# Optimization experiments

Measured on AMD Instinct MI355X. Metric: run time of the kernel, lower is better.

Reference implementation:

```python
import jax, jax.numpy as jnp
import numpy as np

# LIF parameters (norse defaults, matching lif_params in init_kwargs)
TAU_MEM_INV = 100.0
TAU_SYN_INV = 200.0
V_LEAK = 0.0
V_TH = 1.0
V_RESET = 0.0
DT = 0.001
POOL = (2, 2)

B, C, H, W = 16, 64, 256, 256


def setup_inputs() -> dict:
    key = jax.random.key(0)
    input_signal = jax.random.normal(key, (B, C, H, W), dtype=jnp.float32)
    membrane = jnp.zeros((B, C, H, W), dtype=jnp.float32)
    synaptic = jnp.zeros((B, C, H, W), dtype=jnp.float32)
    return {"input_signal": input_signal, "membrane": membrane, "synaptic": synaptic}


def reference(input_signal, membrane, synaptic):
    # Single-timestep LIF update per pixel (Euler integration):
    #   i' = i + dt * tau_syn_inv * (-i) + input
    #   v' = v + dt * tau_mem_inv * ((v_leak - v) + i')
    #   spike = v' >= v_th
    i_new = synaptic * (1.0 - DT * TAU_SYN_INV) + input_signal
    v_new = membrane + DT * TAU_MEM_INV * ((V_LEAK - membrane) + i_new)
    spikes = jnp.where(v_new >= V_TH, 1.0, 0.0).astype(input_signal.dtype)
    # Max-pool the spike map over non-overlapping POOL windows.
    ph, pw = POOL
    b, c, h, w = spikes.shape
    pooled = spikes.reshape(b, c, h // ph, ph, w // pw, pw).max(axis=(3, 5))
    return pooled  # [B, C, H//ph, W//pw]
```

## Files before the change

### kernel.cpp

```cpp
#include <hip/hip_runtime.h>


constexpr int B = 16, C = 64, H = 256, W = 256;
constexpr int OW = W / 2;
constexpr int NROWS = B * C * H;
constexpr int NTHREADS = (NROWS / 2) * (OW / 2);

__global__ __launch_bounds__(256) void lif_pool_kernel(
    const float4* __restrict__ x,
    const float4* __restrict__ m,
    const float4* __restrict__ s,
    float2* __restrict__ out)
{
    int t = blockIdx.x * blockDim.x + threadIdx.x;
    if (t >= NTHREADS) return;

    int orow = t >> 6;
    int ocp  = t & 63;

    int i0 = (2 * orow) * (W / 4) + ocp;
    int i1 = i0 + (W / 4);

    float4 x0 = x[i0], x1 = x[i1];
    float4 m0 = m[i0], m1 = m[i1];
    float4 s0 = s[i0], s1 = s[i1];

    float v00 = fmaf(0.9f, m0.x, 0.1f * fmaf(0.8f, s0.x, x0.x));
    float v01 = fmaf(0.9f, m0.y, 0.1f * fmaf(0.8f, s0.y, x0.y));
    float v02 = fmaf(0.9f, m0.z, 0.1f * fmaf(0.8f, s0.z, x0.z));
    float v03 = fmaf(0.9f, m0.w, 0.1f * fmaf(0.8f, s0.w, x0.w));
    float v10 = fmaf(0.9f, m1.x, 0.1f * fmaf(0.8f, s1.x, x1.x));
    float v11 = fmaf(0.9f, m1.y, 0.1f * fmaf(0.8f, s1.y, x1.y));
    float v12 = fmaf(0.9f, m1.z, 0.1f * fmaf(0.8f, s1.z, x1.z));
    float v13 = fmaf(0.9f, m1.w, 0.1f * fmaf(0.8f, s1.w, x1.w));

    float w0 = fmaxf(fmaxf(v00, v01), fmaxf(v10, v11));
    float w1 = fmaxf(fmaxf(v02, v03), fmaxf(v12, v13));

    float2 o;
    o.x = (w0 >= 1.0f) ? 1.0f : 0.0f;
    o.y = (w1 >= 1.0f) ? 1.0f : 0.0f;

    out[orow * (OW / 2) + ocp] = o;
}

extern "C" void kernel_launch(void* const* d_in, const int* in_sizes, int n_in,
                              void* d_out, int out_size, void* d_ws, size_t ws_size,
                              hipStream_t stream) {
    const float4* x = (const float4*)d_in[0];
    const float4* m = (const float4*)d_in[1];
    const float4* s = (const float4*)d_in[2];
    float2* out = (float2*)d_out;

    constexpr int BLOCK = 256;
    constexpr int GRID = (NTHREADS + BLOCK - 1) / BLOCK;
    lif_pool_kernel<<<GRID, BLOCK, 0, stream>>>(x, m, s, out);
}
```

Measured before the change: 669.7 us.

## Process four input rows per thread with grid-stride loop and nontemporal stores

Each thread now handles a 4-row by 4-column input tile, producing two pooled output rows, which doubles the loads in flight per thread. The launch becomes a fixed 2048-block grid-stride loop with a launch-bounds occupancy hint, and outputs are written with nontemporal stores to avoid polluting cache. The aim is better memory-level parallelism and less per-thread overhead on a purely bandwidth-bound kernel. The costs are higher register use per thread, possibly lower occupancy, and a fixed grid size that may not match the number of CUs.

```diff
diff --git a/kernel.cpp b/kernel.cpp
--- a/kernel.cpp
+++ b/kernel.cpp
@@ -2,46 +2,54 @@
 
 
 constexpr int B = 16, C = 64, H = 256, W = 256;
-constexpr int OW = W / 2;
 constexpr int NROWS = B * C * H;
-constexpr int NTHREADS = (NROWS / 2) * (OW / 2);
+constexpr int ROWF4 = W / 4;
+constexpr int NTILES = (NROWS / 4) * ROWF4;
+constexpr int OWF2 = (W / 2) / 2;
 
-__global__ __launch_bounds__(256) void lif_pool_kernel(
+typedef float vf2 __attribute__((ext_vector_type(2)));
+
+#define LIF(mm, ss, xx) fmaf(0.9f, (mm), 0.1f * fmaf(0.8f, (ss), (xx)))
+
+__global__ __launch_bounds__(256, 8) void lif_pool_kernel(
     const float4* __restrict__ x,
     const float4* __restrict__ m,
     const float4* __restrict__ s,
-    float2* __restrict__ out)
+    vf2* __restrict__ out)
 {
-    int t = blockIdx.x * blockDim.x + threadIdx.x;
-    if (t >= NTHREADS) return;
+    const int stride = gridDim.x * blockDim.x;
+    for (int u = blockIdx.x * blockDim.x + threadIdx.x; u < NTILES; u += stride) {
+        const int rg  = u >> 6;
+        const int ocp = u & 63;
+        const int i0  = rg * (4 * ROWF4) + ocp;
 
-    int orow = t >> 6;
-    int ocp  = t & 63;
+        float4 x0 = x[i0], x1 = x[i0 + ROWF4], x2 = x[i0 + 2 * ROWF4], x3 = x[i0 + 3 * ROWF4];
+        float4 m0 = m[i0], m1 = m[i0 + ROWF4], m2 = m[i0 + 2 * ROWF4], m3 = m[i0 + 3 * ROWF4];
+        float4 s0 = s[i0], s1 = s[i0 + ROWF4], s2 = s[i0 + 2 * ROWF4], s3 = s[i0 + 3 * ROWF4];
 
-    int i0 = (2 * orow) * (W / 4) + ocp;
-    int i1 = i0 + (W / 4);
+        float v00 = LIF(m0.x, s0.x, x0.x), v01 = LIF(m0.y, s0.y, x0.y);
+        float v02 = LIF(m0.z, s0.z, x0.z), v03 = LIF(m0.w, s0.w, x0.w);
+        float v10 = LIF(m1.x, s1.x, x1.x), v11 = LIF(m1.y, s1.y, x1.y);
+        float v12 = LIF(m1.z, s1.z, x1.z), v13 = LIF(m1.w, s1.w, x1.w);
+        float v20 = LIF(m2.x, s2.x, x2.x), v21 = LIF(m2.y, s2.y, x2.y);
+        float v22 = LIF(m2.z, s2.z, x2.z), v23 = LIF(m2.w, s2.w, x2.w);
+        float v30 = LIF(m3.x, s3.x, x3.x), v31 = LIF(m3.y, s3.y, x3.y);
+        float v32 = LIF(m3.z, s3.z, x3.z), v33 = LIF(m3.w, s3.w, x3.w);
 
-    float4 x0 = x[i0], x1 = x[i1];
-    float4 m0 = m[i0], m1 = m[i1];
-    float4 s0 = s[i0], s1 = s[i1];
+        float a0 = fmaxf(fmaxf(v00, v01), fmaxf(v10, v11));
+        float a1 = fmaxf(fmaxf(v02, v03), fmaxf(v12, v13));
+        float b0 = fmaxf(fmaxf(v20, v21), fmaxf(v30, v31));
+        float b1 = fmaxf(fmaxf(v22, v23), fmaxf(v32, v33));
 
-    float v00 = fmaf(0.9f, m0.x, 0.1f * fmaf(0.8f, s0.x, x0.x));
-    float v01 = fmaf(0.9f, m0.y, 0.1f * fmaf(0.8f, s0.y, x0.y));
-    float v02 = fmaf(0.9f, m0.z, 0.1f * fmaf(0.8f, s0.z, x0.z));
-    float v03 = fmaf(0.9f, m0.w, 0.1f * fmaf(0.8f, s0.w, x0.w));
-    float v10 = fmaf(0.9f, m1.x, 0.1f * fmaf(0.8f, s1.x, x1.x));
-    float v11 = fmaf(0.9f, m1.y, 0.1f * fmaf(0.8f, s1.y, x1.y));
-    float v12 = fmaf(0.9f, m1.z, 0.1f * fmaf(0.8f, s1.z, x1.z));
-    float v13 = fmaf(0.9f, m1.w, 0.1f * fmaf(0.8f, s1.w, x1.w));
+        vf2 oa, ob;
+        oa.x = (a0 >= 1.0f) ? 1.0f : 0.0f;
+        oa.y = (a1 >= 1.0f) ? 1.0f : 0.0f;
+        ob.x = (b0 >= 1.0f) ? 1.0f : 0.0f;
+        ob.y = (b1 >= 1.0f) ? 1.0f : 0.0f;
 
-    float w0 = fmaxf(fmaxf(v00, v01), fmaxf(v10, v11));
-    float w1 = fmaxf(fmaxf(v02, v03), fmaxf(v12, v13));
-
-    float2 o;
-    o.x = (w0 >= 1.0f) ? 1.0f : 0.0f;
-    o.y = (w1 >= 1.0f) ? 1.0f : 0.0f;
-
-    out[orow * (OW / 2) + ocp] = o;
+        __builtin_nontemporal_store(oa, &out[(2 * rg)     * OWF2 + ocp]);
+        __builtin_nontemporal_store(ob, &out[(2 * rg + 1) * OWF2 + ocp]);
+    }
 }
 
 extern "C" void kernel_launch(void* const* d_in, const int* in_sizes, int n_in,
@@ -50,9 +58,9 @@
     const float4* x = (const float4*)d_in[0];
     const float4* m = (const float4*)d_in[1];
     const float4* s = (const float4*)d_in[2];
-    float2* out = (float2*)d_out;
+    vf2* out = (vf2*)d_out;
 
     constexpr int BLOCK = 256;
-    constexpr int GRID = (NTHREADS + BLOCK - 1) / BLOCK;
+    constexpr int GRID = 2048;
     lif_pool_kernel<<<GRID, BLOCK, 0, stream>>>(x, m, s, out);
 }
```

New measurement: 674.7 us. No clear change (+0.7%).
